# Kernel tuning notes

Measured on AMD Instinct MI355X. Metric: run time of the kernel, lower is better.

## Reference

```python
import jax, jax.numpy as jnp
import numpy as np

B, S, D = 8, 1024, 1024
H, DK, DV = 16, 64, 64
EPS = 1e-5


def gaussian_prior(n_heads, len_q, len_k):
    # per-head causal Gaussian bias: exp(-(i-j)^2 / (2*sigma_h^2)) for i>=j else 0
    i = jnp.arange(len_q)[:, None]
    j = jnp.arange(len_k)[None, :]
    dist2 = (i - j).astype(jnp.float32) ** 2              # [S, S]
    sigma = jnp.arange(1, n_heads + 1, dtype=jnp.float32) # sigma_h = h+1
    bias = jnp.exp(-dist2[None] / (2.0 * sigma[:, None, None] ** 2))  # [H, S, S]
    return jnp.where(i >= j, bias, 0.0)


def setup_inputs() -> dict:
    key = jax.random.key(0)
    ks = jax.random.split(key, 7)
    input_Q = jax.random.normal(ks[0], (B, S, D), dtype=jnp.float32)
    input_K = jax.random.normal(ks[1], (B, S, D), dtype=jnp.float32)
    input_V = jax.random.normal(ks[2], (B, S, D), dtype=jnp.float32)
    # causal mask: True where attention is disallowed (j > i)
    causal = jnp.triu(jnp.ones((S, S), dtype=bool), k=1)
    attn_mask = jnp.broadcast_to(causal, (B, S, S))
    scale = 0.02
    Wq = jax.random.normal(ks[3], (H * DK, D), dtype=jnp.float32) * scale  # torch Linear weight [out,in]
    Wk = jax.random.normal(ks[4], (H * DK, D), dtype=jnp.float32) * scale
    Wv = jax.random.normal(ks[5], (H * DV, D), dtype=jnp.float32) * scale
    Wfc = jax.random.normal(ks[6], (D, H * DV), dtype=jnp.float32) * scale
    return {"input_Q": input_Q, "input_K": input_K, "input_V": input_V,
            "attn_mask": attn_mask, "Wq": Wq, "Wk": Wk, "Wv": Wv, "Wfc": Wfc}


def reference(input_Q, input_K, input_V, attn_mask, Wq, Wk, Wv, Wfc):
    b, s, d = input_Q.shape
    residual = input_Q
    # projections -> [B, H, S, dk]
    Q = (input_Q @ Wq.T).reshape(b, s, H, DK).transpose(0, 2, 1, 3)
    K = (input_K @ Wk.T).reshape(b, s, H, DK).transpose(0, 2, 1, 3)
    V = (input_V @ Wv.T).reshape(b, s, H, DV).transpose(0, 2, 1, 3)
    scores = jnp.einsum("bhqd,bhkd->bhqk", Q, K) / jnp.sqrt(jnp.float32(DK))
    scores = scores + gaussian_prior(H, s, s)[None]        # add Gaussian positional bias
    scores = jnp.where(attn_mask[:, None], -1e9, scores)   # masked_fill_
    attn = jax.nn.softmax(scores, axis=-1)
    context = jnp.einsum("bhqk,bhkd->bhqd", attn, V)
    context = context.transpose(0, 2, 1, 3).reshape(b, s, H * DV)
    output = context @ Wfc.T
    x = output + residual
    # LayerNorm (fresh module each call in source -> weight=1, bias=0)
    mu = jnp.mean(x, axis=-1, keepdims=True)
    var = jnp.var(x, axis=-1, keepdims=True)
    out = (x - mu) * jax.lax.rsqrt(var + EPS)
    return out, attn
```

## Files before the change

kernel.cpp:

```cpp
#include <hip/hip_runtime.h>
#include <hip/hip_bf16.h>

#define NP 8388608

typedef __attribute__((ext_vector_type(8))) short short8;
typedef __attribute__((ext_vector_type(4))) float f32x4;

__device__ __forceinline__ ushort f2bf(float f) {
  union { float f; unsigned u; } v; v.f = f;
  unsigned r = v.u + 0x7fffu + ((v.u >> 16) & 1u);
  return (ushort)(r >> 16);
}

__device__ __forceinline__ void gload16(const void* g, void* l) {
  __builtin_amdgcn_global_load_lds((const __attribute__((address_space(1))) void*)g,
                                   (__attribute__((address_space(3))) void*)l, 16, 0, 0);
}

__global__ void cast_inputs(const float* __restrict__ a, const float* __restrict__ b,
                            const float* __restrict__ c, ushort* __restrict__ dst) {
  const float* src = (blockIdx.y == 0) ? a : (blockIdx.y == 1) ? b : c;
  ushort* d = dst + (size_t)blockIdx.y * NP;
  size_t i = ((size_t)blockIdx.x * 256 + threadIdx.x) * 4;
  f32x4 v = *(const f32x4*)(src + i);
  ushort4 o; o.x = f2bf(v[0]); o.y = f2bf(v[1]); o.z = f2bf(v[2]); o.w = f2bf(v[3]);
  *(ushort4*)(d + i) = o;
}

__global__ void cast_weights(const float* __restrict__ w0, const float* __restrict__ w1,
                             const float* __restrict__ w2, const float* __restrict__ w3,
                             ushort* __restrict__ dst) {
  const float* src = (blockIdx.y == 0) ? w0 : (blockIdx.y == 1) ? w1
                    : (blockIdx.y == 2) ? w2 : w3;
  ushort* d = dst + (size_t)blockIdx.y * 1048576;
  size_t i = ((size_t)blockIdx.x * 256 + threadIdx.x) * 4;
  f32x4 v = *(const f32x4*)(src + i);
  ushort4 o; o.x = f2bf(v[0]); o.y = f2bf(v[1]); o.z = f2bf(v[2]); o.w = f2bf(v[3]);
  *(ushort4*)(d + i) = o;
}

template<int EPI>
__global__ __launch_bounds__(256) void gemm_bt(const ushort* __restrict__ Abase,
                                               const ushort* __restrict__ Bbase,
                                               float* __restrict__ Cf32,
                                               ushort* __restrict__ Qh,
                                               ushort* __restrict__ Kh,
                                               ushort* __restrict__ VhT) {
  constexpr int K = 1024;
  __shared__ ushort As[4096];
  __shared__ ushort Bs[4096];
  const int t = threadIdx.x, w = t >> 6, l = t & 63;
  const int o  = blockIdx.y * 8 + blockIdx.x;
  const int o2 = (o & 7) * 64 + (o >> 3);
  const int n0 = (o2 & 7) * 128, m0 = (o2 >> 3) * 128;
  const int z = blockIdx.z;
  const ushort* A  = Abase + (EPI == 0 ? (size_t)z * NP : 0);
  const ushort* Bm = Bbase + (EPI == 0 ? (size_t)z * 1048576 : 0);

  f32x4 acc[4][4];
#pragma unroll
  for (int i = 0; i < 4; i++)
#pragma unroll
    for (int j = 0; j < 4; j++) acc[i][j] = f32x4{0.f, 0.f, 0.f, 0.f};

  const int wm = w >> 1, wn = w & 1;
  const int arow = w * 16 + (l >> 2);
  const int acol = (l & 3) * 8;
  const int fr = l & 15, fq = l >> 4, fk = fq * 8;

  for (int k0 = 0; k0 < K; k0 += 32) {
    __syncthreads();
#pragma unroll
    for (int r = 0; r < 2; r++) {
      gload16(A  + (size_t)(m0 + r * 64 + arow) * K + k0 + acol, &As[r * 2048 + w * 512]);
      gload16(Bm + (size_t)(n0 + r * 64 + arow) * K + k0 + acol, &Bs[r * 2048 + w * 512]);
    }
    __syncthreads();
    short8 av[4], bv[4];
#pragma unroll
    for (int i = 0; i < 4; i++) {
      av[i] = *(const short8*)&As[(wm * 64 + i * 16 + fr) * 32 + fk];
      bv[i] = *(const short8*)&Bs[(wn * 64 + i * 16 + fr) * 32 + fk];
    }
#pragma unroll
    for (int i = 0; i < 4; i++)
#pragma unroll
      for (int j = 0; j < 4; j++)
        acc[i][j] = __builtin_amdgcn_mfma_f32_16x16x32_bf16(av[i], bv[j], acc[i][j], 0, 0, 0);
  }

#pragma unroll
  for (int i = 0; i < 4; i++)
#pragma unroll
    for (int j = 0; j < 4; j++)
#pragma unroll
      for (int reg = 0; reg < 4; reg++) {
        int m = m0 + wm * 64 + i * 16 + fq * 4 + reg;
        int n = n0 + wn * 64 + j * 16 + fr;
        float v = acc[i][j][reg];
        if (EPI == 1) {
          Cf32[(size_t)m * 1024 + n] = v;
        } else {
          int b = m >> 10, s = m & 1023, h = n >> 6, d = n & 63;
          if (z == 0)
            Qh[((size_t)(b * 16 + h) * 1024 + s) * 64 + d] = f2bf(v * 0.125f);
          else if (z == 1)
            Kh[((size_t)(b * 16 + h) * 1024 + s) * 64 + d] = f2bf(v);
          else
            VhT[((size_t)(b * 16 + h) * 64 + d) * 1024 + s] = f2bf(v);
        }
      }
}

__global__ __launch_bounds__(256) void attn_fused(const ushort* __restrict__ Qh,
                                                  const ushort* __restrict__ Kh,
                                                  const ushort* __restrict__ VhT,
                                                  float* __restrict__ attnO,
                                                  ushort* __restrict__ ctx) {
  __shared__ ushort Kt[4096];
  __shared__ ushort Vt[4096];
  __shared__ float  biasl[1024];
  __shared__ ushort Pl[4096];

  const int t = threadIdx.x, w = t >> 6, l = t & 63;
  const int o = blockIdx.x + 8 * blockIdx.y + 128 * blockIdx.z;
  const int gx = (o >> 3) & 7;
  const int bhid = (o & 7) + 8 * (o >> 6);
  const int h = bhid & 15, b = bhid >> 4;
  const size_t bh = (size_t)b * 16 + h;
  const int fr = l & 15, fq = l >> 4, fk = fq * 8;

  const float sig = (float)(h + 1);
  const float inv2s2 = 1.0f / (2.0f * sig * sig);
  for (int d = t; d < 1024; d += 256) {
    float fd = (float)d;
    biasl[d] = __expf(-fd * fd * inv2s2);
  }

  const int srow = w * 8 + (l >> 3);
  const int sc = l & 7;
  char* Prow = (char*)(Pl + w * 1024 + fr * 64);
  const int pswz = (fr & 7) << 4;

  for (int half = 0; half < 2; half++) {
    const int qt = half ? 15 - gx : gx;
    const int q0 = qt * 64;
    const int qrow_g = q0 + w * 16 + fr;

    const ushort* qrow = Qh + (bh * 1024 + qrow_g) * 64;
    short8 qa0 = *(const short8*)(qrow + fk);
    short8 qa1 = *(const short8*)(qrow + 32 + fk);

    float psum = 0.f;
    for (int kt = 0; kt <= qt; kt++) {
      __syncthreads();
#pragma unroll
      for (int r = 0; r < 2; r++) {
        int row = r * 32 + srow;
        int col = (sc ^ (row & 7)) * 8;
        gload16(Kh + (bh * 1024 + kt * 64 + row) * 64 + col, &Kt[r * 2048 + w * 512]);
      }
      __syncthreads();
#pragma unroll
      for (int cb = 0; cb < 4; cb++) {
        int krow = cb * 16 + fr;
        short8 kb0 = *(const short8*)&Kt[krow * 64 + ((fq ^ (krow & 7)) * 8)];
        short8 kb1 = *(const short8*)&Kt[krow * 64 + (((fq + 4) ^ (krow & 7)) * 8)];
        f32x4 s = f32x4{0.f, 0.f, 0.f, 0.f};
        s = __builtin_amdgcn_mfma_f32_16x16x32_bf16(kb0, qa0, s, 0, 0, 0);
        s = __builtin_amdgcn_mfma_f32_16x16x32_bf16(kb1, qa1, s, 0, 0, 0);
        int kbase = kt * 64 + cb * 16 + fq * 4;
#pragma unroll
        for (int reg = 0; reg < 4; reg++) {
          int dd = qrow_g - (kbase + reg);
          if (dd >= 0) psum += __expf(s[reg] + biasl[dd]);
        }
      }
    }
    psum += __shfl_xor(psum, 16, 64);
    psum += __shfl_xor(psum, 32, 64);
    const float linv = 1.0f / psum;

    f32x4 cacc[4];
#pragma unroll
    for (int nb = 0; nb < 4; nb++) cacc[nb] = f32x4{0.f, 0.f, 0.f, 0.f};

    float* arow_p = attnO + (bh * 1024 + qrow_g) * 1024;

    for (int kt = 0; kt <= qt; kt++) {
      __syncthreads();
#pragma unroll
      for (int r = 0; r < 2; r++) {
        int row = r * 32 + srow;
        int col = (sc ^ (row & 7)) * 8;
        gload16(Kh  + (bh * 1024 + kt * 64 + row) * 64 + col, &Kt[r * 2048 + w * 512]);
        gload16(VhT + (bh * 64 + row) * 1024 + kt * 64 + col, &Vt[r * 2048 + w * 512]);
      }
      __syncthreads();

#pragma unroll
      for (int cb = 0; cb < 4; cb++) {
        int krow = cb * 16 + fr;
        short8 kb0 = *(const short8*)&Kt[krow * 64 + ((fq ^ (krow & 7)) * 8)];
        short8 kb1 = *(const short8*)&Kt[krow * 64 + (((fq + 4) ^ (krow & 7)) * 8)];
        f32x4 s = f32x4{0.f, 0.f, 0.f, 0.f};
        s = __builtin_amdgcn_mfma_f32_16x16x32_bf16(kb0, qa0, s, 0, 0, 0);
        s = __builtin_amdgcn_mfma_f32_16x16x32_bf16(kb1, qa1, s, 0, 0, 0);
        int kbase = kt * 64 + cb * 16 + fq * 4;
        f32x4 o;
#pragma unroll
        for (int reg = 0; reg < 4; reg++) {
          int dd = qrow_g - (kbase + reg);
          o[reg] = (dd >= 0) ? __expf(s[reg] + biasl[dd]) * linv : 0.0f;
        }
        __builtin_nontemporal_store(o, (f32x4*)(arow_p + kbase));
        uint2 pk;
        pk.x = (unsigned)f2bf(o[0]) | ((unsigned)f2bf(o[1]) << 16);
        pk.y = (unsigned)f2bf(o[2]) | ((unsigned)f2bf(o[3]) << 16);
        *(uint2*)(Prow + (((cb * 32 + fq * 8) ^ pswz))) = pk;
      }

      asm volatile("s_waitcnt lgkmcnt(0)" ::: "memory");
      __builtin_amdgcn_sched_barrier(0);

      short8 pa0 = *(const short8*)(Prow + ((fq * 16) ^ pswz));
      short8 pa1 = *(const short8*)(Prow + ((64 + fq * 16) ^ pswz));
#pragma unroll
      for (int nb = 0; nb < 4; nb++) {
        int vrow = nb * 16 + fr;
        short8 vb0 = *(const short8*)&Vt[vrow * 64 + ((fq ^ (vrow & 7)) * 8)];
        short8 vb1 = *(const short8*)&Vt[vrow * 64 + (((fq + 4) ^ (vrow & 7)) * 8)];
        cacc[nb] = __builtin_amdgcn_mfma_f32_16x16x32_bf16(pa0, vb0, cacc[nb], 0, 0, 0);
        cacc[nb] = __builtin_amdgcn_mfma_f32_16x16x32_bf16(pa1, vb1, cacc[nb], 0, 0, 0);
      }
    }

    int cstart = (qt + 1) * 64;
    if (cstart < 1024) {
      int W4 = (1024 - cstart) >> 2;
      for (int r = w; r < 64; r += 4) {
        float* dst = attnO + (bh * 1024 + q0 + r) * 1024 + cstart;
        for (int c = l; c < W4; c += 64)
          __builtin_nontemporal_store(f32x4{0.f, 0.f, 0.f, 0.f}, (f32x4*)dst + c);
      }
    }

#pragma unroll
    for (int nb = 0; nb < 4; nb++)
#pragma unroll
      for (int reg = 0; reg < 4; reg++) {
        int s = q0 + w * 16 + fq * 4 + reg;
        int col = h * 64 + nb * 16 + fr;
        ctx[((size_t)b * 1024 + s) * 1024 + col] = f2bf(cacc[nb][reg]);
      }
  }
}

__global__ __launch_bounds__(256) void ln_kernel(const float* __restrict__ fc,
                                                 const float* __restrict__ resid,
                                                 float* __restrict__ out) {
  const int row = blockIdx.x, t = threadIdx.x, w = t >> 6, l = t & 63;
  f32x4 xf = *(const f32x4*)(fc    + (size_t)row * 1024 + t * 4);
  f32x4 xr = *(const f32x4*)(resid + (size_t)row * 1024 + t * 4);
  f32x4 x;
#pragma unroll
  for (int i = 0; i < 4; i++) x[i] = xf[i] + xr[i];
  float s1 = x[0] + x[1] + x[2] + x[3];
  float s2 = x[0]*x[0] + x[1]*x[1] + x[2]*x[2] + x[3]*x[3];
#pragma unroll
  for (int off = 1; off < 64; off <<= 1) {
    s1 += __shfl_xor(s1, off, 64);
    s2 += __shfl_xor(s2, off, 64);
  }
  __shared__ float red[8];
  if (l == 0) { red[w] = s1; red[4 + w] = s2; }
  __syncthreads();
  float S1 = red[0] + red[1] + red[2] + red[3];
  float S2 = red[4] + red[5] + red[6] + red[7];
  float mu = S1 * (1.0f / 1024.0f);
  float var = S2 * (1.0f / 1024.0f) - mu * mu;
  float rs = rsqrtf(var + 1e-5f);
  f32x4 o;
#pragma unroll
  for (int i = 0; i < 4; i++) o[i] = (x[i] - mu) * rs;
  *(f32x4*)(out + (size_t)row * 1024 + t * 4) = o;
}

extern "C" void kernel_launch(void* const* d_in, const int* in_sizes, int n_in,
                              void* d_out, int out_size, void* d_ws, size_t ws_size,
                              hipStream_t stream) {
  const float* inQ = (const float*)d_in[0];
  const float* inK = (const float*)d_in[1];
  const float* inV = (const float*)d_in[2];
  const float* Wq  = (const float*)d_in[4];
  const float* Wk  = (const float*)d_in[5];
  const float* Wv  = (const float*)d_in[6];
  const float* Wfc = (const float*)d_in[7];
  float* out   = (float*)d_out;
  float* attnO = out + (size_t)NP;

  char* wsb = (char*)d_ws;
  ushort* Wb   = (ushort*)wsb;
  ushort* inXb = (ushort*)(wsb + 8388608ull);
  ushort* Qh   = (ushort*)(wsb + 58720256ull);
  ushort* Kh   = (ushort*)(wsb + 75497472ull);
  ushort* VhT  = (ushort*)(wsb + 92274688ull);
  ushort* ctx  = (ushort*)(wsb + 8388608ull);
  float*  fcO  = (float*)(wsb + 25165824ull);

  cast_inputs <<<dim3(8192, 3), 256, 0, stream>>>(inQ, inK, inV, inXb);
  cast_weights<<<dim3(1024, 4), 256, 0, stream>>>(Wq, Wk, Wv, Wfc, Wb);
  gemm_bt<0>  <<<dim3(8, 64, 3), 256, 0, stream>>>(inXb, Wb, nullptr, Qh, Kh, VhT);
  attn_fused  <<<dim3(8, 16, 8), 256, 0, stream>>>(Qh, Kh, VhT, attnO, ctx);
  gemm_bt<1>  <<<dim3(8, 64, 1), 256, 0, stream>>>(ctx, Wb + 3145728, fcO,
                                                   nullptr, nullptr, nullptr);
  ln_kernel   <<<8192, 256, 0, stream>>>(fcO, inQ, out);
}
```

Measured before the change: 332.2 us.

## Double-buffer K/V tiles in LDS and compute Gaussian bias inline

Splits the K and V shared-memory tiles into two buffers so the next key tile is prefetched with global_load_lds while the current tile is consumed, replacing two __syncthreads per iteration with vmcnt waits plus a single barrier. It drops the LDS bias table and recomputes the Gaussian bias with an extra exp per score, which frees LDS at the cost of more transcendental work. It also switches the attention-probability stores from nontemporal to ordinary stores, which may change cache behaviour on the large attn output write.

```diff
diff --git a/kernel.cpp b/kernel.cpp
--- a/kernel.cpp
+++ b/kernel.cpp
@@ -117,9 +117,8 @@
                                                   const ushort* __restrict__ VhT,
                                                   float* __restrict__ attnO,
                                                   ushort* __restrict__ ctx) {
-  __shared__ ushort Kt[4096];
-  __shared__ ushort Vt[4096];
-  __shared__ float  biasl[1024];
+  __shared__ ushort Kt[2][4096];
+  __shared__ ushort Vt[2][4096];
   __shared__ ushort Pl[4096];
 
   const int t = threadIdx.x, w = t >> 6, l = t & 63;
@@ -131,41 +130,53 @@
   const int fr = l & 15, fq = l >> 4, fk = fq * 8;
 
   const float sig = (float)(h + 1);
-  const float inv2s2 = 1.0f / (2.0f * sig * sig);
-  for (int d = t; d < 1024; d += 256) {
-    float fd = (float)d;
-    biasl[d] = __expf(-fd * fd * inv2s2);
-  }
+  const float minv = -1.0f / (2.0f * sig * sig);
 
   const int srow = w * 8 + (l >> 3);
   const int sc = l & 7;
   char* Prow = (char*)(Pl + w * 1024 + fr * 64);
   const int pswz = (fr & 7) << 4;
 
+  auto stageK = [&](int kt, int bsel) {
+#pragma unroll
+    for (int r = 0; r < 2; r++) {
+      int row = r * 32 + srow;
+      int col = (sc ^ (row & 7)) * 8;
+      gload16(Kh + (bh * 1024 + kt * 64 + row) * 64 + col, &Kt[bsel][r * 2048 + w * 512]);
+    }
+  };
+  auto stageV = [&](int kt, int bsel) {
+#pragma unroll
+    for (int r = 0; r < 2; r++) {
+      int row = r * 32 + srow;
+      int col = (sc ^ (row & 7)) * 8;
+      gload16(VhT + (bh * 64 + row) * 1024 + kt * 64 + col, &Vt[bsel][r * 2048 + w * 512]);
+    }
+  };
+
   for (int half = 0; half < 2; half++) {
     const int qt = half ? 15 - gx : gx;
     const int q0 = qt * 64;
     const int qrow_g = q0 + w * 16 + fr;
+    const float frow = (float)qrow_g;
 
     const ushort* qrow = Qh + (bh * 1024 + qrow_g) * 64;
     short8 qa0 = *(const short8*)(qrow + fk);
     short8 qa1 = *(const short8*)(qrow + 32 + fk);
 
     float psum = 0.f;
+    stageK(0, 0);
+    asm volatile("s_waitcnt vmcnt(0)" ::: "memory");
+    __builtin_amdgcn_s_barrier();
     for (int kt = 0; kt <= qt; kt++) {
-      __syncthreads();
-#pragma unroll
-      for (int r = 0; r < 2; r++) {
-        int row = r * 32 + srow;
-        int col = (sc ^ (row & 7)) * 8;
-        gload16(Kh + (bh * 1024 + kt * 64 + row) * 64 + col, &Kt[r * 2048 + w * 512]);
-      }
-      __syncthreads();
+      const int cur = kt & 1;
+      if (kt < qt) stageK(kt + 1, cur ^ 1);
+      __builtin_amdgcn_sched_barrier(0);
 #pragma unroll
       for (int cb = 0; cb < 4; cb++) {
         int krow = cb * 16 + fr;
-        short8 kb0 = *(const short8*)&Kt[krow * 64 + ((fq ^ (krow & 7)) * 8)];
-        short8 kb1 = *(const short8*)&Kt[krow * 64 + (((fq + 4) ^ (krow & 7)) * 8)];
+        short8 kb0 = *(const short8*)&Kt[cur][krow * 64 + ((fq ^ (krow & 7)) * 8)];
+        short8 kb1 = *(const short8*)&Kt[cur][krow * 64 + (((fq + 4) ^ (krow & 7)) * 8)];
         f32x4 s = f32x4{0.f, 0.f, 0.f, 0.f};
         s = __builtin_amdgcn_mfma_f32_16x16x32_bf16(kb0, qa0, s, 0, 0, 0);
         s = __builtin_amdgcn_mfma_f32_16x16x32_bf16(kb1, qa1, s, 0, 0, 0);
@@ -173,9 +184,14 @@
 #pragma unroll
         for (int reg = 0; reg < 4; reg++) {
           int dd = qrow_g - (kbase + reg);
-          if (dd >= 0) psum += __expf(s[reg] + biasl[dd]);
+          float fd = (float)dd;
+          float bb = __expf(fd * fd * minv);
+          float p = __expf(s[reg] + bb);
+          if (dd >= 0) psum += p;
         }
       }
+      asm volatile("s_waitcnt vmcnt(0)" ::: "memory");
+      __builtin_amdgcn_s_barrier();
     }
     psum += __shfl_xor(psum, 16, 64);
     psum += __shfl_xor(psum, 32, 64);
@@ -187,22 +203,19 @@
 
     float* arow_p = attnO + (bh * 1024 + qrow_g) * 1024;
 
+    stageK(0, 0); stageV(0, 0);
+    asm volatile("s_waitcnt vmcnt(0)" ::: "memory");
+    __builtin_amdgcn_s_barrier();
     for (int kt = 0; kt <= qt; kt++) {
-      __syncthreads();
-#pragma unroll
-      for (int r = 0; r < 2; r++) {
-        int row = r * 32 + srow;
-        int col = (sc ^ (row & 7)) * 8;
-        gload16(Kh  + (bh * 1024 + kt * 64 + row) * 64 + col, &Kt[r * 2048 + w * 512]);
-        gload16(VhT + (bh * 64 + row) * 1024 + kt * 64 + col, &Vt[r * 2048 + w * 512]);
-      }
-      __syncthreads();
+      const int cur = kt & 1;
+      if (kt < qt) { stageK(kt + 1, cur ^ 1); stageV(kt + 1, cur ^ 1); }
+      __builtin_amdgcn_sched_barrier(0);
 
 #pragma unroll
       for (int cb = 0; cb < 4; cb++) {
         int krow = cb * 16 + fr;
-        short8 kb0 = *(const short8*)&Kt[krow * 64 + ((fq ^ (krow & 7)) * 8)];
-        short8 kb1 = *(const short8*)&Kt[krow * 64 + (((fq + 4) ^ (krow & 7)) * 8)];
+        short8 kb0 = *(const short8*)&Kt[cur][krow * 64 + ((fq ^ (krow & 7)) * 8)];
+        short8 kb1 = *(const short8*)&Kt[cur][krow * 64 + (((fq + 4) ^ (krow & 7)) * 8)];
         f32x4 s = f32x4{0.f, 0.f, 0.f, 0.f};
         s = __builtin_amdgcn_mfma_f32_16x16x32_bf16(kb0, qa0, s, 0, 0, 0);
         s = __builtin_amdgcn_mfma_f32_16x16x32_bf16(kb1, qa1, s, 0, 0, 0);
@@ -211,9 +224,12 @@
 #pragma unroll
         for (int reg = 0; reg < 4; reg++) {
           int dd = qrow_g - (kbase + reg);
-          o[reg] = (dd >= 0) ? __expf(s[reg] + biasl[dd]) * linv : 0.0f;
+          float fd = (float)dd;
+          float bb = __expf(fd * fd * minv);
+          float p = __expf(s[reg] + bb) * linv;
+          o[reg] = (dd >= 0) ? p : 0.0f;
         }
-        __builtin_nontemporal_store(o, (f32x4*)(arow_p + kbase));
+        *(f32x4*)(arow_p + kbase) = o;
         uint2 pk;
         pk.x = (unsigned)f2bf(o[0]) | ((unsigned)f2bf(o[1]) << 16);
         pk.y = (unsigned)f2bf(o[2]) | ((unsigned)f2bf(o[3]) << 16);
@@ -228,11 +244,14 @@
 #pragma unroll
       for (int nb = 0; nb < 4; nb++) {
         int vrow = nb * 16 + fr;
-        short8 vb0 = *(const short8*)&Vt[vrow * 64 + ((fq ^ (vrow & 7)) * 8)];
-        short8 vb1 = *(const short8*)&Vt[vrow * 64 + (((fq + 4) ^ (vrow & 7)) * 8)];
+        short8 vb0 = *(const short8*)&Vt[cur][vrow * 64 + ((fq ^ (vrow & 7)) * 8)];
+        short8 vb1 = *(const short8*)&Vt[cur][vrow * 64 + (((fq + 4) ^ (vrow & 7)) * 8)];
         cacc[nb] = __builtin_amdgcn_mfma_f32_16x16x32_bf16(pa0, vb0, cacc[nb], 0, 0, 0);
         cacc[nb] = __builtin_amdgcn_mfma_f32_16x16x32_bf16(pa1, vb1, cacc[nb], 0, 0, 0);
       }
+
+      asm volatile("s_waitcnt vmcnt(4)" ::: "memory");
+      __builtin_amdgcn_s_barrier();
     }
 
     int cstart = (qt + 1) * 64;
```

Measured after the change: 316.1 us. 1.05x faster.
